# Optimization experiments

Measured on AMD Instinct MI355X. Metric: run time of the kernel, lower is better.

Reference implementation:

```python
import jax, jax.numpy as jnp
import numpy as np

B, S, E, H = 64, 197, 768, 12
HD = E // H  # 64


def setup_inputs() -> dict:
    key = jax.random.key(0)
    ks = jax.random.split(key, 9)
    sd = 0.02
    return {
        "x": jax.random.normal(ks[0], (B, S, E), dtype=jnp.float32),
        "Wq": jax.random.normal(ks[1], (E, E), dtype=jnp.float32) * sd,
        "bq": jax.random.normal(ks[2], (E,), dtype=jnp.float32) * sd,
        "Wk": jax.random.normal(ks[3], (E, E), dtype=jnp.float32) * sd,
        "bk": jax.random.normal(ks[4], (E,), dtype=jnp.float32) * sd,
        "Wv": jax.random.normal(ks[5], (E, E), dtype=jnp.float32) * sd,
        "bv": jax.random.normal(ks[6], (E,), dtype=jnp.float32) * sd,
        "Wp": jax.random.normal(ks[7], (E, E), dtype=jnp.float32) * sd,
        "bp": jax.random.normal(ks[8], (E,), dtype=jnp.float32) * sd,
    }


def reference(x, Wq, bq, Wk, bk, Wv, bv, Wp, bp):
    # nn.Linear: y = x @ W.T + b
    Q = x @ Wq.T + bq
    K = x @ Wk.T + bk
    V = x @ Wv.T + bv
    # Faithful to original: plain view (reshape) WITHOUT transpose.
    # (B, S, E) -> (B, H, S, HD): heads index contiguous chunks of the
    # flattened (S*E) memory, exactly as torch .view does.
    Q = Q.reshape(B, H, S, HD)
    K = K.reshape(B, H, S, HD)
    V = V.reshape(B, H, S, HD)
    energy = jnp.einsum("bhqd,bhkd->bhqk", Q, K)  # [B,H,S,S]
    scale = jnp.float32(E) ** 0.5
    # Faithful quirk: softmax FIRST, then divide by sqrt(emb_size).
    att = jax.nn.softmax(energy, axis=-1) / scale
    out = jnp.einsum("bhqk,bhkd->bhqd", att, V)  # [B,H,S,HD]
    out = out.reshape(B, S, E)
    return out @ Wp.T + bp
```

## Files before the change

### kernel.cpp

```cpp
#include <hip/hip_runtime.h>
#include <stdint.h>

#define BSZ 64
#define SEQ 197
#define EMB 768
#define NH  12
#define HD  64
#define M_TOK (BSZ*SEQ)
#define SHD (SEQ*HD)

using bf16x8 = __attribute__((ext_vector_type(8))) short;
using f32x4  = __attribute__((ext_vector_type(4))) float;

__device__ __forceinline__ float bflo(uint32_t u) { return __uint_as_float(u << 16); }
__device__ __forceinline__ uint16_t f2bf(float f) {
    uint32_t u = __float_as_uint(f);
    u += 0x7fffu + ((u >> 16) & 1u);
    return (uint16_t)(u >> 16);
}

struct CvtJob { const float* src; uint16_t* dst; int n8; };
struct CvtJobs { CvtJob j[9]; };

__global__ __launch_bounds__(256) void convert_kernel(CvtJobs jobs)
{
    int idx = blockIdx.x * 256 + threadIdx.x;
    #pragma unroll
    for (int r = 0; r < 9; ++r) {
        const int n8 = jobs.j[r].n8;
        if (idx < n8) {
            const uint4* s4 = (const uint4*)(jobs.j[r].src + (size_t)idx * 8);
            uint4 a = s4[0], b = s4[1];
            uint4 w;
            w.x = (uint32_t)f2bf(__uint_as_float(a.x)) | ((uint32_t)f2bf(__uint_as_float(a.y)) << 16);
            w.y = (uint32_t)f2bf(__uint_as_float(a.z)) | ((uint32_t)f2bf(__uint_as_float(a.w)) << 16);
            w.z = (uint32_t)f2bf(__uint_as_float(b.x)) | ((uint32_t)f2bf(__uint_as_float(b.y)) << 16);
            w.w = (uint32_t)f2bf(__uint_as_float(b.z)) | ((uint32_t)f2bf(__uint_as_float(b.w)) << 16);
            *(uint4*)(jobs.j[r].dst + (size_t)idx * 8) = w;
            return;
        }
        idx -= n8;
    }
}

struct GemmPtrs {
    const uint16_t* W[3];
    const uint16_t* b[3];
    void*           out[3];
};

__global__ __launch_bounds__(256) void gemm_bias_nt(const uint16_t* __restrict__ A,
                                                    GemmPtrs p, int M,
                                                    int total, int nz, int outf32)
{
    __shared__ __align__(16) uint16_t sA[2][128 * 32];
    __shared__ __align__(16) uint16_t sB[2][128 * 32];

    const int flat  = blockIdx.x;
    const int xcd   = flat & 7;
    const int local = flat >> 3;
    const int cb = total >> 3, r8 = total & 7;
    const int start = xcd * cb + (xcd < r8 ? xcd : r8);
    const int wid = start + local;
    const int per_m = 6 * nz;
    const int m_idx = wid / per_m;
    const int rem   = wid - m_idx * per_m;
    const int z     = rem / 6;
    const int n_idx = rem - z * 6;

    const uint16_t* __restrict__ W    = p.W[z];
    const uint16_t* __restrict__ bias = p.b[z];

    const int m0   = m_idx * 128;
    const int n0   = n_idx * 128;
    const int tid  = threadIdx.x;
    const int lane = tid & 63;
    const int wave = tid >> 6;
    const int wr = wave >> 1, wc = wave & 1;
    const int l15 = lane & 15;
    const int kq  = lane >> 6 ? 0 : lane >> 4;

    const int c0 = tid, c1 = tid + 256;
    const int row0 = c0 >> 2, kc0 = c0 & 3;
    const int row1 = c1 >> 2, kc1 = c1 & 3;
    const int ks0 = (kc0 ^ ((row0 >> 1) & 3)) * 8;
    const int ks1 = (kc1 ^ ((row1 >> 1) & 3)) * 8;
    int ga0 = m0 + row0; if (ga0 >= M) ga0 = M - 1;
    int ga1 = m0 + row1; if (ga1 >= M) ga1 = M - 1;
    const uint16_t* a0p = A + (size_t)ga0 * EMB + ks0;
    const uint16_t* a1p = A + (size_t)ga1 * EMB + ks1;
    const uint16_t* b0p = W + (size_t)(n0 + row0) * EMB + ks0;
    const uint16_t* b1p = W + (size_t)(n0 + row1) * EMB + ks1;

    const int kqs = ((lane >> 4) ^ ((l15 >> 1) & 3)) * 8;

    f32x4 acc[4][4] = {};

    #define STAGE(buf, k0)                                                        \
        do {                                                                      \
            __builtin_amdgcn_global_load_lds(                                     \
                (const __attribute__((address_space(1))) void*)(a0p + (k0)),      \
                (__attribute__((address_space(3))) void*)(sA[buf] + c0 * 8), 16, 0, 0); \
            __builtin_amdgcn_global_load_lds(                                     \
                (const __attribute__((address_space(1))) void*)(a1p + (k0)),      \
                (__attribute__((address_space(3))) void*)(sA[buf] + c1 * 8), 16, 0, 0); \
            __builtin_amdgcn_global_load_lds(                                     \
                (const __attribute__((address_space(1))) void*)(b0p + (k0)),      \
                (__attribute__((address_space(3))) void*)(sB[buf] + c0 * 8), 16, 0, 0); \
            __builtin_amdgcn_global_load_lds(                                     \
                (const __attribute__((address_space(1))) void*)(b1p + (k0)),      \
                (__attribute__((address_space(3))) void*)(sB[buf] + c1 * 8), 16, 0, 0); \
        } while (0)

    STAGE(0, 0);

    const int NIT = EMB / 32;
    for (int it = 0; it < NIT; ++it) {
        const int cur = it & 1;
        if (it + 1 < NIT) {
            STAGE(cur ^ 1, (it + 1) * 32);
            asm volatile("s_waitcnt vmcnt(4)" ::: "memory");
        } else {
            asm volatile("s_waitcnt vmcnt(0)" ::: "memory");
        }
        __builtin_amdgcn_s_barrier();
        asm volatile("" ::: "memory");

        bf16x8 af[4], bfr[4];
        #pragma unroll
        for (int i = 0; i < 4; ++i)
            af[i] = *(const bf16x8*)(sA[cur] + (64 * wr + 16 * i + l15) * 32 + kqs);
        #pragma unroll
        for (int j = 0; j < 4; ++j)
            bfr[j] = *(const bf16x8*)(sB[cur] + (64 * wc + 16 * j + l15) * 32 + kqs);

        #pragma unroll
        for (int i = 0; i < 4; ++i)
            #pragma unroll
            for (int j = 0; j < 4; ++j)
                acc[i][j] = __builtin_amdgcn_mfma_f32_16x16x32_bf16(af[i], bfr[j], acc[i][j], 0, 0, 0);

        asm volatile("s_waitcnt lgkmcnt(0)" ::: "memory");
        __builtin_amdgcn_s_barrier();
        asm volatile("" ::: "memory");
    }
    #undef STAGE

    const int kq4 = (lane >> 4) * 4;
    #pragma unroll
    for (int j = 0; j < 4; ++j) {
        int n = n0 + 64 * wc + 16 * j + l15;
        float bv = bflo((uint32_t)bias[n]);
        #pragma unroll
        for (int i = 0; i < 4; ++i) {
            #pragma unroll
            for (int r = 0; r < 4; ++r) {
                int m = m0 + 64 * wr + 16 * i + kq4 + r;
                if (m < M) {
                    float v = acc[i][j][r] + bv;
                    if (outf32) ((float*)p.out[z])[(size_t)m * EMB + n] = v;
                    else        ((uint16_t*)p.out[z])[(size_t)m * EMB + n] = f2bf(v);
                }
            }
        }
    }
}

#define RV 264
#define RP 72
__global__ __launch_bounds__(256) void attn_kernel(const uint16_t* __restrict__ Qg,
                                                   const uint16_t* __restrict__ Kg,
                                                   const uint16_t* __restrict__ Vg,
                                                   uint16_t* __restrict__ Og)
{
    __shared__ __align__(16) uint16_t sVt[HD * RV];
    __shared__ __align__(16) uint16_t sP[4][64 * RP];

    const int bh  = blockIdx.x;
    const size_t base = (size_t)bh * SHD;
    const int tid  = threadIdx.x;
    const int lane = tid & 63;
    const int w    = tid >> 6;
    const int l15  = lane & 15;
    const int kq   = lane >> 4;
    uint16_t* sPw = sP[w];

    {
        int r = tid >> 2, t4 = tid & 3;
        for (int c = SEQ + t4; c < RV; c += 4) sVt[r * RV + c] = 0;
    }
    for (int idx = tid; idx < SHD / 8; idx += 256) {
        int key = idx >> 3, dc = idx & 7;
        uint4 v = ((const uint4*)(Vg + base))[idx];
        uint16_t e[8];
        *(uint4*)e = v;
        #pragma unroll
        for (int j = 0; j < 8; ++j) sVt[(dc * 8 + j) * RV + key] = e[j];
    }

    bf16x8 aq[4][2];
    #pragma unroll
    for (int mi = 0; mi < 4; ++mi) {
        int m = 64 * w + 16 * mi + l15; if (m >= SEQ) m = SEQ - 1;
        const uint16_t* qp = Qg + base + (size_t)m * HD + kq * 8;
        aq[mi][0] = *(const bf16x8*)(qp);
        aq[mi][1] = *(const bf16x8*)(qp + 32);
    }

    bf16x8 ones;
    #pragma unroll
    for (int j = 0; j < 8; ++j) ones[j] = (short)0x3F80;

    f32x4 oacc[4][4] = {};
    f32x4 lacc[4]    = {};

    __syncthreads();

    for (int c = 0; c < 4; ++c) {
        bf16x8 bk[4][2];
        #pragma unroll
        for (int ni = 0; ni < 4; ++ni) {
            int key = 64 * c + 16 * ni + l15; if (key >= SEQ) key = SEQ - 1;
            const uint16_t* kp = Kg + base + (size_t)key * HD + kq * 8;
            bk[ni][0] = *(const bf16x8*)(kp);
            bk[ni][1] = *(const bf16x8*)(kp + 32);
        }
        #pragma unroll
        for (int mi = 0; mi < 4; ++mi) {
            #pragma unroll
            for (int ni = 0; ni < 4; ++ni) {
                f32x4 s = {};
                s = __builtin_amdgcn_mfma_f32_16x16x32_bf16(aq[mi][0], bk[ni][0], s, 0, 0, 0);
                s = __builtin_amdgcn_mfma_f32_16x16x32_bf16(aq[mi][1], bk[ni][1], s, 0, 0, 0);
                int col = 16 * ni + l15;
                int key = 64 * c + col;
                #pragma unroll
                for (int r = 0; r < 4; ++r) {
                    float pv = (key < SEQ) ? __expf(fminf(s[r], 80.f)) : 0.f;
                    sPw[(16 * mi + kq * 4 + r) * RP + col] = f2bf(pv);
                }
            }
        }

        bf16x8 bv[2][4];
        #pragma unroll
        for (int kk = 0; kk < 2; ++kk)
            #pragma unroll
            for (int ni = 0; ni < 4; ++ni)
                bv[kk][ni] = *(const bf16x8*)(sVt + (16 * ni + l15) * RV + c * 64 + kk * 32 + kq * 8);

        #pragma unroll
        for (int mi = 0; mi < 4; ++mi) {
            #pragma unroll
            for (int kk = 0; kk < 2; ++kk) {
                bf16x8 ap = *(const bf16x8*)(sPw + (16 * mi + l15) * RP + kk * 32 + kq * 8);
                lacc[mi] = __builtin_amdgcn_mfma_f32_16x16x32_bf16(ap, ones, lacc[mi], 0, 0, 0);
                #pragma unroll
                for (int ni = 0; ni < 4; ++ni)
                    oacc[mi][ni] = __builtin_amdgcn_mfma_f32_16x16x32_bf16(ap, bv[kk][ni], oacc[mi][ni], 0, 0, 0);
            }
        }
    }

    #pragma unroll
    for (int mi = 0; mi < 4; ++mi) {
        #pragma unroll
        for (int r = 0; r < 4; ++r) {
            int m = 64 * w + 16 * mi + kq * 4 + r;
            if (m < SEQ) {
                float scale = 1.f / (lacc[mi][r] * 27.712812921102035f);
                #pragma unroll
                for (int ni = 0; ni < 4; ++ni)
                    Og[base + (size_t)m * HD + 16 * ni + l15] = f2bf(oacc[mi][ni][r] * scale);
            }
        }
    }
}

extern "C" void kernel_launch(void* const* d_in, const int* in_sizes, int n_in,
                              void* d_out, int out_size, void* d_ws, size_t ws_size,
                              hipStream_t stream)
{
    const size_t NX = (size_t)M_TOK * EMB;
    const size_t NW = (size_t)EMB * EMB;
    const size_t NB = EMB;

    uint16_t* xbf = (uint16_t*)d_ws;
    uint16_t* Wbf[4]; uint16_t* bbf[4];
    uint16_t* cur = xbf + NX;
    for (int i = 0; i < 4; ++i) { Wbf[i] = cur; cur += NW; }
    for (int i = 0; i < 4; ++i) { bbf[i] = cur; cur += NB; }
    uint16_t* Qw = cur;
    uint16_t* Kw = Qw + NX;
    uint16_t* Vw = Kw + NX;

    const size_t need_primary  = 2 * (NX + 4 * NW + 4 * NB + 3 * NX);
    const size_t need_fallback = need_primary - 2 * NX;
    if (ws_size < need_fallback) return;
    if (ws_size < need_primary) Vw = (uint16_t*)d_out;

    CvtJobs jobs;
    jobs.j[0] = { (const float*)d_in[0], xbf,    (int)(NX / 8) };
    jobs.j[1] = { (const float*)d_in[1], Wbf[0], (int)(NW / 8) };
    jobs.j[2] = { (const float*)d_in[3], Wbf[1], (int)(NW / 8) };
    jobs.j[3] = { (const float*)d_in[5], Wbf[2], (int)(NW / 8) };
    jobs.j[4] = { (const float*)d_in[7], Wbf[3], (int)(NW / 8) };
    jobs.j[5] = { (const float*)d_in[2], bbf[0], (int)(NB / 8) };
    jobs.j[6] = { (const float*)d_in[4], bbf[1], (int)(NB / 8) };
    jobs.j[7] = { (const float*)d_in[6], bbf[2], (int)(NB / 8) };
    jobs.j[8] = { (const float*)d_in[8], bbf[3], (int)(NB / 8) };
    const int total8 = (int)((NX + 4 * NW + 4 * NB) / 8);
    convert_kernel<<<(total8 + 255) / 256, 256, 0, stream>>>(jobs);

    const int MT = (M_TOK + 127) / 128;

    GemmPtrs qkv;
    qkv.W[0] = Wbf[0]; qkv.W[1] = Wbf[1]; qkv.W[2] = Wbf[2];
    qkv.b[0] = bbf[0]; qkv.b[1] = bbf[1]; qkv.b[2] = bbf[2];
    qkv.out[0] = Qw; qkv.out[1] = Kw; qkv.out[2] = Vw;
    const int tot1 = MT * 6 * 3;
    gemm_bias_nt<<<tot1, 256, 0, stream>>>(xbf, qkv, M_TOK, tot1, 3, 0);

    attn_kernel<<<dim3(BSZ * NH), 256, 0, stream>>>(Qw, Kw, Vw, Qw);

    GemmPtrs pr;
    pr.W[0] = pr.W[1] = pr.W[2] = Wbf[3];
    pr.b[0] = pr.b[1] = pr.b[2] = bbf[3];
    pr.out[0] = pr.out[1] = pr.out[2] = d_out;
    const int tot2 = MT * 6 * 1;
    gemm_bias_nt<<<tot2, 256, 0, stream>>>(Qw, pr, M_TOK, tot2, 1, 1);
}
```

Measured before the change: 264.8 us.

## Load GEMM A fragments directly from global into registers, staging only B in LDS

The GEMM no longer stages the A tile through shared memory. Each wave loads its A MFMA fragments straight from global memory into registers, prefetching the next k-step, while only the weight tile is double-buffered in LDS. This halves LDS footprint and LDS traffic, drops one barrier per iteration, and adds a launch_bounds occupancy hint of 3 blocks. The costs are uncoalesced 16-byte global loads for A, duplicated A reads across the two column waves, and a full vmcnt(0) wait each iteration that may expose load latency.

```diff
diff --git a/kernel.cpp b/kernel.cpp
--- a/kernel.cpp
+++ b/kernel.cpp
@@ -49,61 +49,55 @@
     void*           out[3];
 };
 
-__global__ __launch_bounds__(256) void gemm_bias_nt(const uint16_t* __restrict__ A,
-                                                    GemmPtrs p, int M,
-                                                    int total, int nz, int outf32)
+__global__ __launch_bounds__(256, 3) void gemm_bias_nt(const uint16_t* __restrict__ A,
+                                                       GemmPtrs p, int M,
+                                                       int total, int per_m, int outf32)
 {
-    __shared__ __align__(16) uint16_t sA[2][128 * 32];
     __shared__ __align__(16) uint16_t sB[2][128 * 32];
 
     const int flat  = blockIdx.x;
     const int xcd   = flat & 7;
     const int local = flat >> 3;
-    const int cb = total >> 3, r8 = total & 7;
-    const int start = xcd * cb + (xcd < r8 ? xcd : r8);
+    const int cbk = total >> 3, r8 = total & 7;
+    const int start = xcd * cbk + (xcd < r8 ? xcd : r8);
     const int wid = start + local;
-    const int per_m = 6 * nz;
     const int m_idx = wid / per_m;
-    const int rem   = wid - m_idx * per_m;
-    const int z     = rem / 6;
-    const int n_idx = rem - z * 6;
+    const int nt    = wid - m_idx * per_m;
+    const int z     = nt / 6;
+    const int n0    = (nt - z * 6) * 128;
 
     const uint16_t* __restrict__ W    = p.W[z];
     const uint16_t* __restrict__ bias = p.b[z];
 
     const int m0   = m_idx * 128;
-    const int n0   = n_idx * 128;
     const int tid  = threadIdx.x;
     const int lane = tid & 63;
     const int wave = tid >> 6;
     const int wr = wave >> 1, wc = wave & 1;
     const int l15 = lane & 15;
-    const int kq  = lane >> 6 ? 0 : lane >> 4;
+    const int kq  = lane >> 4;
 
     const int c0 = tid, c1 = tid + 256;
     const int row0 = c0 >> 2, kc0 = c0 & 3;
     const int row1 = c1 >> 2, kc1 = c1 & 3;
     const int ks0 = (kc0 ^ ((row0 >> 1) & 3)) * 8;
     const int ks1 = (kc1 ^ ((row1 >> 1) & 3)) * 8;
-    int ga0 = m0 + row0; if (ga0 >= M) ga0 = M - 1;
-    int ga1 = m0 + row1; if (ga1 >= M) ga1 = M - 1;
-    const uint16_t* a0p = A + (size_t)ga0 * EMB + ks0;
-    const uint16_t* a1p = A + (size_t)ga1 * EMB + ks1;
     const uint16_t* b0p = W + (size_t)(n0 + row0) * EMB + ks0;
     const uint16_t* b1p = W + (size_t)(n0 + row1) * EMB + ks1;
 
-    const int kqs = ((lane >> 4) ^ ((l15 >> 1) & 3)) * 8;
+    const int kqs = (kq ^ ((l15 >> 1) & 3)) * 8;
+
+    const uint16_t* a_ptr[4];
+    #pragma unroll
+    for (int i = 0; i < 4; ++i) {
+        int m = m0 + 64 * wr + 16 * i + l15; if (m >= M) m = M - 1;
+        a_ptr[i] = A + (size_t)m * EMB + kq * 8;
+    }
 
     f32x4 acc[4][4] = {};
 
-    #define STAGE(buf, k0)                                                        \
+    #define STAGE_B(buf, k0)                                                      \
         do {                                                                      \
-            __builtin_amdgcn_global_load_lds(                                     \
-                (const __attribute__((address_space(1))) void*)(a0p + (k0)),      \
-                (__attribute__((address_space(3))) void*)(sA[buf] + c0 * 8), 16, 0, 0); \
-            __builtin_amdgcn_global_load_lds(                                     \
-                (const __attribute__((address_space(1))) void*)(a1p + (k0)),      \
-                (__attribute__((address_space(3))) void*)(sA[buf] + c1 * 8), 16, 0, 0); \
             __builtin_amdgcn_global_load_lds(                                     \
                 (const __attribute__((address_space(1))) void*)(b0p + (k0)),      \
                 (__attribute__((address_space(3))) void*)(sB[buf] + c0 * 8), 16, 0, 0); \
@@ -112,24 +106,25 @@
                 (__attribute__((address_space(3))) void*)(sB[buf] + c1 * 8), 16, 0, 0); \
         } while (0)
 
-    STAGE(0, 0);
+    bf16x8 afc[4], afn[4];
+    #pragma unroll
+    for (int i = 0; i < 4; ++i) afc[i] = *(const bf16x8*)(a_ptr[i]);
+    STAGE_B(0, 0);
 
     const int NIT = EMB / 32;
     for (int it = 0; it < NIT; ++it) {
         const int cur = it & 1;
-        if (it + 1 < NIT) {
-            STAGE(cur ^ 1, (it + 1) * 32);
-            asm volatile("s_waitcnt vmcnt(4)" ::: "memory");
-        } else {
-            asm volatile("s_waitcnt vmcnt(0)" ::: "memory");
-        }
+        asm volatile("s_waitcnt vmcnt(0)" ::: "memory");
         __builtin_amdgcn_s_barrier();
         asm volatile("" ::: "memory");
-
-        bf16x8 af[4], bfr[4];
-        #pragma unroll
-        for (int i = 0; i < 4; ++i)
-            af[i] = *(const bf16x8*)(sA[cur] + (64 * wr + 16 * i + l15) * 32 + kqs);
+        if (it + 1 < NIT) {
+            STAGE_B(cur ^ 1, (it + 1) * 32);
+            #pragma unroll
+            for (int i = 0; i < 4; ++i)
+                afn[i] = *(const bf16x8*)(a_ptr[i] + (it + 1) * 32);
+        }
+
+        bf16x8 bfr[4];
         #pragma unroll
         for (int j = 0; j < 4; ++j)
             bfr[j] = *(const bf16x8*)(sB[cur] + (64 * wc + 16 * j + l15) * 32 + kqs);
@@ -138,15 +133,14 @@
         for (int i = 0; i < 4; ++i)
             #pragma unroll
             for (int j = 0; j < 4; ++j)
-                acc[i][j] = __builtin_amdgcn_mfma_f32_16x16x32_bf16(af[i], bfr[j], acc[i][j], 0, 0, 0);
-
-        asm volatile("s_waitcnt lgkmcnt(0)" ::: "memory");
-        __builtin_amdgcn_s_barrier();
-        asm volatile("" ::: "memory");
-    }
-    #undef STAGE
-
-    const int kq4 = (lane >> 4) * 4;
+                acc[i][j] = __builtin_amdgcn_mfma_f32_16x16x32_bf16(afc[i], bfr[j], acc[i][j], 0, 0, 0);
+
+        #pragma unroll
+        for (int i = 0; i < 4; ++i) afc[i] = afn[i];
+    }
+    #undef STAGE_B
+
+    const int kq4 = kq * 4;
     #pragma unroll
     for (int j = 0; j < 4; ++j) {
         int n = n0 + 64 * wc + 16 * j + l15;
@@ -318,8 +312,8 @@
     qkv.W[0] = Wbf[0]; qkv.W[1] = Wbf[1]; qkv.W[2] = Wbf[2];
     qkv.b[0] = bbf[0]; qkv.b[1] = bbf[1]; qkv.b[2] = bbf[2];
     qkv.out[0] = Qw; qkv.out[1] = Kw; qkv.out[2] = Vw;
-    const int tot1 = MT * 6 * 3;
-    gemm_bias_nt<<<tot1, 256, 0, stream>>>(xbf, qkv, M_TOK, tot1, 3, 0);
+    const int tot1 = MT * 18;
+    gemm_bias_nt<<<tot1, 256, 0, stream>>>(xbf, qkv, M_TOK, tot1, 18, 0);
 
     attn_kernel<<<dim3(BSZ * NH), 256, 0, stream>>>(Qw, Kw, Vw, Qw);
 
@@ -327,6 +321,6 @@
     pr.W[0] = pr.W[1] = pr.W[2] = Wbf[3];
     pr.b[0] = pr.b[1] = pr.b[2] = bbf[3];
     pr.out[0] = pr.out[1] = pr.out[2] = d_out;
-    const int tot2 = MT * 6 * 1;
-    gemm_bias_nt<<<tot2, 256, 0, stream>>>(Qw, pr, M_TOK, tot2, 1, 1);
-}
+    const int tot2 = MT * 6;
+    gemm_bias_nt<<<tot2, 256, 0, stream>>>(Qw, pr, M_TOK, tot2, 6, 1);
+}
```

New measurement: 301.0 us. 13.7% more time.
